# Kernel optimization log

Measured on AMD Instinct MI355X. Metric: run time of the kernel, lower is better.

## Reference

```python
import jax, jax.numpy as jnp
import numpy as np

B, NPG = 128, 128          # graphs, nodes per graph
N = B * NPG                # total nodes
K = 16                     # kNN neighbors within cutoff
D = 256                    # embedding_depth
H, DH = 4, 32              # heads = num_layers, head dim = (D//2)//H
L = 4                      # num graph convolutions
NR = 50                    # num_radial
CUTOFF = 2.0
OUT = 3 + 100              # 3 + max_ntypes


def setup_inputs() -> dict:
    rng = np.random.default_rng(0)
    pos = rng.standard_normal((N, 3)).astype(np.float32)
    nbrs = np.zeros((N, K), np.int32)
    mask = np.zeros((N, K), np.float32)
    for g in range(B):  # per-graph kNN with radial cutoff (setup only, numpy)
        p = pos[g * NPG:(g + 1) * NPG]
        d2 = ((p[:, None, :] - p[None, :, :]) ** 2).sum(-1)
        np.fill_diagonal(d2, np.inf)
        idx = np.argsort(d2, axis=1)[:, :K]
        dk = np.sqrt(np.take_along_axis(d2, idx, 1))
        nbrs[g * NPG:(g + 1) * NPG] = idx + g * NPG
        mask[g * NPG:(g + 1) * NPG] = (dk <= CUTOFF).astype(np.float32)
    batch_idx = np.repeat(np.arange(B, dtype=np.int32), NPG)

    key = jax.random.key(0)
    ks = jax.random.split(key, 12)
    s = 0.02
    return {
        'encoding': jax.random.normal(ks[0], (B, D), jnp.float32),
        'pos': jnp.asarray(pos),
        'batch_idx': jnp.asarray(batch_idx),
        'neighbors': jnp.asarray(nbrs),
        'nbr_mask': jnp.asarray(mask),
        'W_in': jax.random.normal(ks[1], (D + 3, D), jnp.float32) * s,
        'b_in': jnp.zeros((D,), jnp.float32),
        'Wq': jax.random.normal(ks[2], (L, D, H * DH), jnp.float32) * s,
        'Wk': jax.random.normal(ks[3], (L, D, H * DH), jnp.float32) * s,
        'Wv': jax.random.normal(ks[4], (L, D, H * DH), jnp.float32) * s,
        'We': jax.random.normal(ks[5], (L, NR, H * DH), jnp.float32) * s,
        'Wo': jax.random.normal(ks[6], (L, H * DH, D), jnp.float32) * s,
        'bo': jnp.zeros((L, D), jnp.float32),
        'Wfc': jax.random.normal(ks[7], (L, D, D), jnp.float32) * s,
        'bfc': jnp.zeros((L, D), jnp.float32),
        'ln_g': jnp.ones((L, D), jnp.float32),
        'ln_b': jnp.zeros((L, D), jnp.float32),
        'W_out': jax.random.normal(ks[8], (D, OUT), jnp.float32) * s,
        'b_out': jnp.zeros((OUT,), jnp.float32),
    }


def reference(encoding, pos, batch_idx, neighbors, nbr_mask,
              W_in, b_in, Wq, Wk, Wv, We, Wo, bo, Wfc, bfc,
              ln_g, ln_b, W_out, b_out):
    # x = encoding.repeat_interleave(graph_sizes); x[:, 0] = 1
    x = encoding[batch_idx]                      # [N, D]
    x = x.at[:, 0].set(1.0)
    h = jnp.concatenate([x, pos], axis=-1) @ W_in + b_in   # concat pos, embed

    # gaussian radial basis of neighbor distances
    dvec = pos[neighbors] - pos[:, None, :]      # [N, K, 3]
    d = jnp.sqrt((dvec ** 2).sum(-1) + 1e-12)    # [N, K]
    centers = jnp.linspace(0.0, CUTOFF, NR)
    width = centers[1] - centers[0]
    rbf = jnp.exp(-0.5 * ((d[..., None] - centers) / width) ** 2)  # [N, K, NR]

    scale = 1.0 / jnp.sqrt(jnp.float32(DH))
    m = nbr_mask[..., None]                      # [N, K, 1]
    for l in range(L):                           # TransformerConv layers
        q = (h @ Wq[l]).reshape(N, H, DH)
        k = (h @ Wk[l]).reshape(N, H, DH)
        v = (h @ Wv[l]).reshape(N, H, DH)
        e = (rbf @ We[l]).reshape(N, K, H, DH)   # edge embedding
        kj = k[neighbors] + e                    # [N, K, H, DH]
        vj = v[neighbors] + e
        logits = jnp.einsum('nhd,nkhd->nkh', q, kj) * scale
        logits = jnp.where(m > 0, logits, -1e9)
        a = jax.nn.softmax(logits, axis=1) * m   # masked attention over K
        msg = jnp.einsum('nkh,nkhd->nhd', a, vj).reshape(N, H * DH)
        h = h + msg @ Wo[l] + bo[l]              # residual update
        mu = h.mean(-1, keepdims=True)
        var = h.var(-1, keepdims=True)
        h = ln_g[l] * (h - mu) / jnp.sqrt(var + 1e-5) + ln_b[l]
        h = jax.nn.gelu(h @ Wfc[l] + bfc[l])     # nodewise fc (1 layer)

    return h @ W_out + b_out                     # [N, 3 + max_ntypes]
```

## Files before the change

### kernel.cpp

```cpp
#include <hip/hip_runtime.h>
#include <hip/hip_bf16.h>
#include <math.h>

#define N_PTS 16384
#define NLAYER 4

typedef __attribute__((ext_vector_type(8))) short bfrag;
typedef __attribute__((ext_vector_type(4))) float f32x4;
typedef __attribute__((ext_vector_type(4))) unsigned short u16x4;
typedef unsigned short ushort_t;
typedef unsigned int uint_t;

__device__ __forceinline__ ushort_t f2b(float f) {
  __hip_bfloat16 h = __float2bfloat16(f);
  return *reinterpret_cast<const ushort_t*>(&h);
}
__device__ __forceinline__ float b2f(ushort_t u) {
  union { uint_t i; float f; } c; c.i = ((uint_t)u) << 16; return c.f;
}
__device__ __forceinline__ float blo(uint_t u) {
  union { uint_t i; float f; } c; c.i = u << 16; return c.f;
}
__device__ __forceinline__ float bhi(uint_t u) {
  union { uint_t i; float f; } c; c.i = u & 0xffff0000u; return c.f;
}

__global__ __launch_bounds__(256) void base_kernel(
    const float* __restrict__ enc, const float* __restrict__ W_in,
    const float* __restrict__ b_in, float* __restrict__ base)
{
  int b = blockIdx.x, j = threadIdx.x;
  __shared__ float se[256];
  se[j] = enc[b * 256 + j];
  __syncthreads();
  float acc = b_in[j] + W_in[j];
  for (int i = 1; i < 256; ++i) acc += se[i] * W_in[i * 256 + j];
  base[b * 256 + j] = acc;
}

__global__ __launch_bounds__(256) void embed_kernel(
    const float* __restrict__ base, const int* __restrict__ batch_idx,
    const float* __restrict__ pos, const float* __restrict__ W_in,
    float* __restrict__ h, ushort_t* __restrict__ h_bf)
{
  int n = blockIdx.x, j = threadIdx.x;
  int b = batch_idx[n];
  float px = pos[n * 3 + 0], py = pos[n * 3 + 1], pz = pos[n * 3 + 2];
  float v = base[b * 256 + j]
      + px * W_in[256 * 256 + j] + py * W_in[257 * 256 + j] + pz * W_in[258 * 256 + j];
  h[(size_t)n * 256 + j] = v;
  h_bf[(size_t)n * 256 + j] = f2b(v);
}

__global__ __launch_bounds__(256) void prep_qkv(
    const float* __restrict__ Wq, const float* __restrict__ Wk,
    const float* __restrict__ Wv, const float* __restrict__ We,
    ushort_t* __restrict__ out)
{
  int idx = blockIdx.x * 256 + threadIdx.x;
  int l = idx / (640 * 256);
  int rem = idx - l * (640 * 256);
  int j = rem >> 8, k = rem & 255;
  float v = 0.f;
  if (j < 128) v = Wq[((size_t)l * 256 + k) * 128 + j];
  else if (j < 328) {
    int p = j - 128, hq = p / 50, r = p - hq * 50;
    const float* wq = &Wq[((size_t)l * 256 + k) * 128 + hq * 32];
    const float* we = &We[((size_t)l * 50 + r) * 128 + hq * 32];
#pragma unroll
    for (int d = 0; d < 32; ++d) v += wq[d] * we[d];
  } else if (j < 456) v = Wk[((size_t)l * 256 + k) * 128 + (j - 328)];
  else if (j < 584) v = Wv[((size_t)l * 256 + k) * 128 + (j - 456)];
  out[idx] = f2b(v);
}

__global__ __launch_bounds__(256) void prep_bcat(
    const float* __restrict__ We, const float* __restrict__ Wo, ushort_t* __restrict__ out)
{
  int idx = blockIdx.x * 256 + threadIdx.x;
  if (idx >= 4 * 256 * 352) return;
  int l = idx / (256 * 352);
  int rem = idx - l * (256 * 352);
  int j = rem / 352, k2 = rem - j * 352;
  float v = 0.f;
  if (k2 < 128) v = Wo[((size_t)l * 128 + k2) * 256 + j];
  else if (k2 < 328) {
    int p = k2 - 128, hq = p / 50, r = p - hq * 50;
    const float* we = &We[((size_t)l * 50 + r) * 128 + hq * 32];
    const float* wo = &Wo[((size_t)l * 128 + hq * 32) * 256 + j];
#pragma unroll
    for (int d = 0; d < 32; ++d) v += we[d] * wo[(size_t)d * 256];
  }
  out[idx] = f2b(v);
}

__global__ __launch_bounds__(256) void prep_wfc(
    const float* __restrict__ Wfc, ushort_t* __restrict__ out)
{
  int idx = blockIdx.x * 256 + threadIdx.x;
  int l = idx >> 16, rem = idx & 65535;
  int j = rem >> 8, k = rem & 255;
  out[idx] = f2b(Wfc[((size_t)l * 256 + k) * 256 + j]);
}

__global__ __launch_bounds__(256) void prep_wout(
    const float* __restrict__ W_out, ushort_t* __restrict__ out)
{
  int idx = blockIdx.x * 256 + threadIdx.x;
  int j = idx >> 8, k = idx & 255;
  out[idx] = (j < 103) ? f2b(W_out[(size_t)k * 103 + j]) : (ushort_t)0;
}

template<int EPI>
__global__ __launch_bounds__(256) void gemm_bf16(
    const ushort_t* __restrict__ A, const ushort_t* __restrict__ BT,
    const float* __restrict__ bias, const float* __restrict__ resid,
    float* __restrict__ Cf, ushort_t* __restrict__ Cb, ushort_t* __restrict__ Cb2,
    int K)
{
  __shared__ __align__(16) short As[128 * 40];
  __shared__ __align__(16) short Bs[64 * 40];
  const int tid = threadIdx.x;
  const int m0 = blockIdx.x * 128, n0 = blockIdx.y * 64;
  const int lane = tid & 63, wv = tid >> 6;
  const int wm = wv >> 1, wn = wv & 1;
  const int l15 = lane & 15, l4 = lane >> 4;
  const int asr = tid >> 1, asc = tid & 1;
  const int bsr = tid >> 2, bsc = tid & 3;

  f32x4 acc[4][2];
#pragma unroll
  for (int i = 0; i < 4; ++i)
#pragma unroll
    for (int j = 0; j < 2; ++j) acc[i][j] = (f32x4){0.f, 0.f, 0.f, 0.f};

  const ushort_t* gA = A + (size_t)(m0 + asr) * K + asc * 16;
  const ushort_t* gB = BT + (size_t)(n0 + bsr) * K + bsc * 8;
  short* wAs = As + asr * 40 + asc * 16;
  short* wBs = Bs + bsr * 40 + bsc * 8;

  for (int k0 = 0; k0 < K; k0 += 32) {
    *(bfrag*)wAs       = *(const bfrag*)(gA + k0);
    *(bfrag*)(wAs + 8) = *(const bfrag*)(gA + k0 + 8);
    *(bfrag*)wBs       = *(const bfrag*)(gB + k0);
    __syncthreads();
    bfrag af[4], bf[2];
#pragma unroll
    for (int m = 0; m < 4; ++m)
      af[m] = *(const bfrag*)(As + (wm * 64 + m * 16 + l15) * 40 + l4 * 8);
#pragma unroll
    for (int nn = 0; nn < 2; ++nn)
      bf[nn] = *(const bfrag*)(Bs + (wn * 32 + nn * 16 + l15) * 40 + l4 * 8);
#pragma unroll
    for (int m = 0; m < 4; ++m)
#pragma unroll
      for (int nn = 0; nn < 2; ++nn)
        acc[m][nn] = __builtin_amdgcn_mfma_f32_16x16x32_bf16(af[m], bf[nn], acc[m][nn], 0, 0, 0);
    __syncthreads();
  }

#pragma unroll
  for (int m = 0; m < 4; ++m) {
    const int rbase = m0 + wm * 64 + m * 16 + l4 * 4;
#pragma unroll
    for (int nn = 0; nn < 2; ++nn) {
      const int c = n0 + wn * 32 + nn * 16 + l15;
#pragma unroll
      for (int i = 0; i < 4; ++i) {
        const int r = rbase + i;
        float v = acc[m][nn][i];
        if (EPI == 0) {
          if (c < 328) Cb[(size_t)r * 328 + c] = f2b(v);
          else if (c < 584) Cb2[(size_t)r * 256 + (c - 328)] = f2b(v);
        } else if (EPI == 1) {
          if (c < 103) Cf[(size_t)r * 103 + c] = v + bias[c];
        } else if (EPI == 2) {
          Cf[(size_t)r * 256 + c] = v + bias[c] + resid[(size_t)r * 256 + c];
        } else {
          float x = v + bias[c];
          float t = tanhf(0.7978845608028654f * (x + 0.044715f * x * x * x));
          float gl = 0.5f * x * (1.f + t);
          Cf[(size_t)r * 256 + c] = gl;
          Cb[(size_t)r * 256 + c] = f2b(gl);
        }
      }
    }
  }
}

__global__ __launch_bounds__(512) void attn_kernel(
    const ushort_t* __restrict__ qext, const ushort_t* __restrict__ kvb,
    const float* __restrict__ pos, const int* __restrict__ nbrs,
    const float* __restrict__ mask, ushort_t* __restrict__ Amsg)
{
  __shared__ ushort_t sKV[128 * 264];
  __shared__ float sPos[128 * 3];
  __shared__ ushort_t sQ[8][336];
  __shared__ float sRbf[8][16][52];
  __shared__ float sA[8][64];
  __shared__ float sD[8][16];
  __shared__ float sMk[8][16];
  __shared__ int   sRn[8][16];

  const int tid = threadIdx.x;
  const int lane = tid & 63, w = tid >> 6;
  const int g = blockIdx.x >> 1, half = blockIdx.x & 1;
  const int base_pt = g * 128;

  for (int e = tid; e < 128 * 32; e += 512) {
    int r = e >> 5, c8 = e & 31;
    uint4 v = *(const uint4*)(kvb + ((size_t)(base_pt + r)) * 256 + c8 * 8);
    *(uint4*)(&sKV[r * 264 + c8 * 8]) = v;
  }
  for (int e = tid; e < 384; e += 512) sPos[e] = pos[(size_t)base_pt * 3 + e];
  __syncthreads();

  const int kk = lane >> 2, hh = lane & 3;
  for (int it = 0; it < 8; ++it) {
    const int rl = half * 64 + w * 8 + it;
    const int n = base_pt + rl;
    if (lane < 16) {
      int nb = nbrs[n * 16 + lane];
      int rn = nb - base_pt;
      sRn[w][lane] = rn;
      sMk[w][lane] = mask[n * 16 + lane];
      float dx = sPos[rn * 3 + 0] - sPos[rl * 3 + 0];
      float dy = sPos[rn * 3 + 1] - sPos[rl * 3 + 1];
      float dz = sPos[rn * 3 + 2] - sPos[rl * 3 + 2];
      sD[w][lane] = sqrtf(dx * dx + dy * dy + dz * dz + 1e-12f);
    }
    if (lane < 41)
      *(uint4*)(&sQ[w][lane * 8]) = *(const uint4*)(qext + (size_t)n * 328 + lane * 8);
    {
      int kk2 = lane & 15;
      float dk = sD[w][kk2];
      int r0 = lane >> 4;
#pragma unroll
      for (int j = 0; j < 13; ++j) {
        int r = r0 + j * 4;
        if (r < 50) {
          float t = (dk - (2.f / 49.f) * (float)r) * 24.5f;
          sRbf[w][kk2][r] = expf(-0.5f * t * t);
        }
      }
    }
    int rn = sRn[w][kk];
    const ushort_t* krow = &sKV[rn * 264 + hh * 32];
    float qk = 0.f;
#pragma unroll
    for (int c8 = 0; c8 < 4; ++c8) {
      uint4 kv4 = *(const uint4*)(krow + c8 * 8);
      const uint_t* q4 = (const uint_t*)(&sQ[w][hh * 32 + c8 * 8]);
      uint_t qa = q4[0], qb = q4[1], qc = q4[2], qd = q4[3];
      qk += blo(qa) * blo(kv4.x) + bhi(qa) * bhi(kv4.x)
          + blo(qb) * blo(kv4.y) + bhi(qb) * bhi(kv4.y)
          + blo(qc) * blo(kv4.z) + bhi(qc) * bhi(kv4.z)
          + blo(qd) * blo(kv4.w) + bhi(qd) * bhi(kv4.w);
    }
    float qe = 0.f;
#pragma unroll
    for (int r = 0; r < 50; ++r) qe += sRbf[w][kk][r] * b2f(sQ[w][128 + hh * 50 + r]);
    float lg = 0.17677669529663687f * (qk + qe);
    lg = (sMk[w][kk] > 0.f) ? lg : -1e9f;

    float mx = lg;
#pragma unroll
    for (int off = 4; off < 64; off <<= 1) mx = fmaxf(mx, __shfl_xor(mx, off, 64));
    float ex = expf(lg - mx);
    float sm = ex;
#pragma unroll
    for (int off = 4; off < 64; off <<= 1) sm += __shfl_xor(sm, off, 64);
    sA[w][kk * 4 + hh] = ex / sm * sMk[w][kk];

#pragma unroll
    for (int h2 = 0; h2 < 4; ++h2) {
      if (lane < 50) {
        float a2 = 0.f;
#pragma unroll
        for (int k2 = 0; k2 < 16; ++k2) a2 += sA[w][k2 * 4 + h2] * sRbf[w][k2][lane];
        Amsg[(size_t)n * 352 + 128 + h2 * 50 + lane] = f2b(a2);
      }
    }
#pragma unroll
    for (int hf = 0; hf < 2; ++hf) {
      int df = lane + hf * 64;
      int h2 = df >> 5;
      float a2 = 0.f;
#pragma unroll
      for (int k2 = 0; k2 < 16; ++k2)
        a2 += sA[w][k2 * 4 + h2] * b2f(sKV[sRn[w][k2] * 264 + 128 + df]);
      Amsg[(size_t)n * 352 + df] = f2b(a2);
    }
    if (lane < 24) Amsg[(size_t)n * 352 + 328 + lane] = 0;
  }
}

__global__ __launch_bounds__(256) void ln_bf(
    const float* __restrict__ h, const float* __restrict__ g,
    const float* __restrict__ b, ushort_t* __restrict__ out)
{
  int row = blockIdx.x * 4 + (threadIdx.x >> 6);
  int lane = threadIdx.x & 63;
  float4 x = *(const float4*)(h + (size_t)row * 256 + lane * 4);
  float s = x.x + x.y + x.z + x.w;
  float ss = x.x * x.x + x.y * x.y + x.z * x.z + x.w * x.w;
#pragma unroll
  for (int off = 1; off < 64; off <<= 1) {
    s += __shfl_xor(s, off, 64);
    ss += __shfl_xor(ss, off, 64);
  }
  float mu = s * (1.f / 256.f);
  float var = ss * (1.f / 256.f) - mu * mu;
  float inv = 1.0f / sqrtf(var + 1e-5f);
  float4 gg = *(const float4*)(g + lane * 4);
  float4 bb = *(const float4*)(b + lane * 4);
  u16x4 o;
  o.x = f2b(gg.x * (x.x - mu) * inv + bb.x);
  o.y = f2b(gg.y * (x.y - mu) * inv + bb.y);
  o.z = f2b(gg.z * (x.z - mu) * inv + bb.z);
  o.w = f2b(gg.w * (x.w - mu) * inv + bb.w);
  *(u16x4*)(out + (size_t)row * 256 + lane * 4) = o;
}

extern "C" void kernel_launch(void* const* d_in, const int* in_sizes, int n_in,
                              void* d_out, int out_size, void* d_ws, size_t ws_size,
                              hipStream_t stream) {
  const float* enc    = (const float*)d_in[0];
  const float* pos    = (const float*)d_in[1];
  const int*   bidx   = (const int*)  d_in[2];
  const int*   nbrs   = (const int*)  d_in[3];
  const float* mask   = (const float*)d_in[4];
  const float* W_in   = (const float*)d_in[5];
  const float* b_in   = (const float*)d_in[6];
  const float* Wq     = (const float*)d_in[7];
  const float* Wk     = (const float*)d_in[8];
  const float* Wv     = (const float*)d_in[9];
  const float* We     = (const float*)d_in[10];
  const float* Wo     = (const float*)d_in[11];
  const float* bo     = (const float*)d_in[12];
  const float* Wfc    = (const float*)d_in[13];
  const float* bfc    = (const float*)d_in[14];
  const float* ln_g   = (const float*)d_in[15];
  const float* ln_b   = (const float*)d_in[16];
  const float* W_out  = (const float*)d_in[17];
  const float* b_out  = (const float*)d_in[18];
  float* out = (float*)d_out;

  const int N = N_PTS;
  float* ws = (float*)d_ws;
  float*    h      = ws;
  ushort_t* qext_b = (ushort_t*)(h + (size_t)N * 256);
  ushort_t* kvb    = qext_b + (size_t)N * 328;
  ushort_t* hln    = kvb;
  ushort_t* h_bf   = kvb + (size_t)N * 256;
  ushort_t* Amsg   = h_bf + (size_t)N * 256;
  float*    base   = (float*)(Amsg + (size_t)N * 352);
  ushort_t* WqkvT  = (ushort_t*)(base + 128 * 256);
  ushort_t* BcT    = WqkvT + 4 * 640 * 256;
  ushort_t* WfT    = BcT  + 4 * 256 * 352;
  ushort_t* WoT    = WfT  + 4 * 256 * 256;

  base_kernel<<<128, 256, 0, stream>>>(enc, W_in, b_in, base);
  embed_kernel<<<N, 256, 0, stream>>>(base, bidx, pos, W_in, h, h_bf);
  prep_qkv<<<(4 * 640 * 256) / 256, 256, 0, stream>>>(Wq, Wk, Wv, We, WqkvT);
  prep_bcat<<<(4 * 256 * 352 + 255) / 256, 256, 0, stream>>>(We, Wo, BcT);
  prep_wfc<<<(4 * 256 * 256) / 256, 256, 0, stream>>>(Wfc, WfT);
  prep_wout<<<(128 * 256) / 256, 256, 0, stream>>>(W_out, WoT);

  for (int l = 0; l < NLAYER; ++l) {
    const ushort_t* WqkvT_l = WqkvT + (size_t)l * 640 * 256;
    const ushort_t* BcT_l   = BcT   + (size_t)l * 256 * 352;
    const ushort_t* WfT_l   = WfT   + (size_t)l * 256 * 256;
    const float* bo_l  = bo  + (size_t)l * 256;
    const float* bfc_l = bfc + (size_t)l * 256;
    const float* lg_l  = ln_g + (size_t)l * 256;
    const float* lb_l  = ln_b + (size_t)l * 256;

    gemm_bf16<0><<<dim3(N / 128, 10), 256, 0, stream>>>(
        h_bf, WqkvT_l, nullptr, nullptr, nullptr, qext_b, kvb, 256);

    attn_kernel<<<256, 512, 0, stream>>>(qext_b, kvb, pos, nbrs, mask, Amsg);

    gemm_bf16<2><<<dim3(N / 128, 4), 256, 0, stream>>>(
        Amsg, BcT_l, bo_l, h, h, nullptr, nullptr, 352);

    ln_bf<<<N / 4, 256, 0, stream>>>(h, lg_l, lb_l, hln);

    gemm_bf16<3><<<dim3(N / 128, 4), 256, 0, stream>>>(
        hln, WfT_l, bfc_l, nullptr, h, h_bf, nullptr, 256);
  }

  gemm_bf16<1><<<dim3(N / 128, 2), 256, 0, stream>>>(
      h_bf, WoT, b_out, nullptr, out, nullptr, nullptr, 256);
}
```

Before: 401.2 us.

## Widen GEMM tiles with direct-to-LDS loads and restructure attention into two phases

The GEMM now uses 128x128 tiles with global_load_lds 16-byte loads straight into unpadded shared memory, halving grid columns so each A tile is reused across more output columns. The attention kernel is split across four blocks per graph, staging K first and then V in a smaller shared buffer, and stores RBF values in bf16. It also uses fast __expf and vectorized q·e dot products. Larger per-block LDS reuse is traded against fewer blocks, unpadded LDS rows that may cause bank conflicts, and bf16 rounding of the RBF terms.

```diff
diff --git a/kernel.cpp b/kernel.cpp
--- a/kernel.cpp
+++ b/kernel.cpp
@@ -23,6 +23,12 @@
 }
 __device__ __forceinline__ float bhi(uint_t u) {
   union { uint_t i; float f; } c; c.i = u & 0xffff0000u; return c.f;
+}
+
+__device__ __forceinline__ void gload16(const ushort_t* g, ushort_t* l) {
+  __builtin_amdgcn_global_load_lds(
+      (const __attribute__((address_space(1))) unsigned int*)g,
+      (__attribute__((address_space(3))) unsigned int*)l, 16, 0, 0);
 }
 
 __global__ __launch_bounds__(256) void base_kernel(
@@ -118,43 +124,48 @@
     float* __restrict__ Cf, ushort_t* __restrict__ Cb, ushort_t* __restrict__ Cb2,
     int K)
 {
-  __shared__ __align__(16) short As[128 * 40];
-  __shared__ __align__(16) short Bs[64 * 40];
+  __shared__ __align__(16) ushort_t As[128 * 32];
+  __shared__ __align__(16) ushort_t Bs[128 * 32];
   const int tid = threadIdx.x;
-  const int m0 = blockIdx.x * 128, n0 = blockIdx.y * 64;
+  const int m0 = blockIdx.x * 128, n0 = blockIdx.y * 128;
   const int lane = tid & 63, wv = tid >> 6;
   const int wm = wv >> 1, wn = wv & 1;
   const int l15 = lane & 15, l4 = lane >> 4;
-  const int asr = tid >> 1, asc = tid & 1;
-  const int bsr = tid >> 2, bsc = tid & 3;
-
-  f32x4 acc[4][2];
+
+  const int srow = wv * 16 + (lane >> 2);
+  const int skc = (lane & 3) << 3;
+  const ushort_t* gA0 = A + (size_t)(m0 + srow) * K + skc;
+  const ushort_t* gA1 = gA0 + (size_t)64 * K;
+  const ushort_t* gB0 = BT + (size_t)(n0 + srow) * K + skc;
+  const ushort_t* gB1 = gB0 + (size_t)64 * K;
+  ushort_t* lA0 = As + wv * 512;
+  ushort_t* lA1 = As + 2048 + wv * 512;
+  ushort_t* lB0 = Bs + wv * 512;
+  ushort_t* lB1 = Bs + 2048 + wv * 512;
+
+  f32x4 acc[4][4];
 #pragma unroll
   for (int i = 0; i < 4; ++i)
 #pragma unroll
-    for (int j = 0; j < 2; ++j) acc[i][j] = (f32x4){0.f, 0.f, 0.f, 0.f};
-
-  const ushort_t* gA = A + (size_t)(m0 + asr) * K + asc * 16;
-  const ushort_t* gB = BT + (size_t)(n0 + bsr) * K + bsc * 8;
-  short* wAs = As + asr * 40 + asc * 16;
-  short* wBs = Bs + bsr * 40 + bsc * 8;
+    for (int j = 0; j < 4; ++j) acc[i][j] = (f32x4){0.f, 0.f, 0.f, 0.f};
 
   for (int k0 = 0; k0 < K; k0 += 32) {
-    *(bfrag*)wAs       = *(const bfrag*)(gA + k0);
-    *(bfrag*)(wAs + 8) = *(const bfrag*)(gA + k0 + 8);
-    *(bfrag*)wBs       = *(const bfrag*)(gB + k0);
+    gload16(gA0 + k0, lA0);
+    gload16(gA1 + k0, lA1);
+    gload16(gB0 + k0, lB0);
+    gload16(gB1 + k0, lB1);
     __syncthreads();
-    bfrag af[4], bf[2];
+    bfrag af[4], bf[4];
 #pragma unroll
     for (int m = 0; m < 4; ++m)
-      af[m] = *(const bfrag*)(As + (wm * 64 + m * 16 + l15) * 40 + l4 * 8);
-#pragma unroll
-    for (int nn = 0; nn < 2; ++nn)
-      bf[nn] = *(const bfrag*)(Bs + (wn * 32 + nn * 16 + l15) * 40 + l4 * 8);
+      af[m] = *(const bfrag*)(As + (wm * 64 + m * 16 + l15) * 32 + l4 * 8);
+#pragma unroll
+    for (int nn = 0; nn < 4; ++nn)
+      bf[nn] = *(const bfrag*)(Bs + (wn * 64 + nn * 16 + l15) * 32 + l4 * 8);
 #pragma unroll
     for (int m = 0; m < 4; ++m)
 #pragma unroll
-      for (int nn = 0; nn < 2; ++nn)
+      for (int nn = 0; nn < 4; ++nn)
         acc[m][nn] = __builtin_amdgcn_mfma_f32_16x16x32_bf16(af[m], bf[nn], acc[m][nn], 0, 0, 0);
     __syncthreads();
   }
@@ -163,8 +174,8 @@
   for (int m = 0; m < 4; ++m) {
     const int rbase = m0 + wm * 64 + m * 16 + l4 * 4;
 #pragma unroll
-    for (int nn = 0; nn < 2; ++nn) {
-      const int c = n0 + wn * 32 + nn * 16 + l15;
+    for (int nn = 0; nn < 4; ++nn) {
+      const int c = n0 + wn * 64 + nn * 16 + l15;
 #pragma unroll
       for (int i = 0; i < 4; ++i) {
         const int r = rbase + i;
@@ -193,44 +204,58 @@
     const float* __restrict__ pos, const int* __restrict__ nbrs,
     const float* __restrict__ mask, ushort_t* __restrict__ Amsg)
 {
-  __shared__ ushort_t sKV[128 * 264];
-  __shared__ float sPos[128 * 3];
-  __shared__ ushort_t sQ[8][336];
-  __shared__ float sRbf[8][16][52];
-  __shared__ float sA[8][64];
-  __shared__ float sD[8][16];
-  __shared__ float sMk[8][16];
-  __shared__ int   sRn[8][16];
+  __shared__ ushort_t sKV[128 * 136];
+  __shared__ float    sPos[384];
+  __shared__ float    sA[32][64];
+  __shared__ int      sRnAll[32][16];
+  __shared__ ushort_t sQ[8][128];
+  __shared__ float    sQE[8][4][52];
+  __shared__ ushort_t sRbf[8][16][52];
+  __shared__ float    sD[8][16];
+  __shared__ float    sMk[8][16];
 
   const int tid = threadIdx.x;
   const int lane = tid & 63, w = tid >> 6;
-  const int g = blockIdx.x >> 1, half = blockIdx.x & 1;
+  const int g = blockIdx.x & 127, q = blockIdx.x >> 7;
   const int base_pt = g * 128;
-
-  for (int e = tid; e < 128 * 32; e += 512) {
-    int r = e >> 5, c8 = e & 31;
-    uint4 v = *(const uint4*)(kvb + ((size_t)(base_pt + r)) * 256 + c8 * 8);
-    *(uint4*)(&sKV[r * 264 + c8 * 8]) = v;
+  const int kk = lane >> 2, hh = lane & 3;
+
+  for (int e = tid; e < 128 * 16; e += 512) {
+    int r = e >> 4, c8 = e & 15;
+    *(uint4*)(&sKV[r * 136 + c8 * 8]) =
+        *(const uint4*)(kvb + (size_t)(base_pt + r) * 256 + c8 * 8);
   }
   for (int e = tid; e < 384; e += 512) sPos[e] = pos[(size_t)base_pt * 3 + e];
   __syncthreads();
 
-  const int kk = lane >> 2, hh = lane & 3;
-  for (int it = 0; it < 8; ++it) {
-    const int rl = half * 64 + w * 8 + it;
+  for (int it = 0; it < 4; ++it) {
+    const int pt = w * 4 + it;
+    const int rl = q * 32 + pt;
     const int n = base_pt + rl;
     if (lane < 16) {
       int nb = nbrs[n * 16 + lane];
       int rn = nb - base_pt;
-      sRn[w][lane] = rn;
+      sRnAll[pt][lane] = rn;
       sMk[w][lane] = mask[n * 16 + lane];
       float dx = sPos[rn * 3 + 0] - sPos[rl * 3 + 0];
       float dy = sPos[rn * 3 + 1] - sPos[rl * 3 + 1];
       float dz = sPos[rn * 3 + 2] - sPos[rl * 3 + 2];
       sD[w][lane] = sqrtf(dx * dx + dy * dy + dz * dz + 1e-12f);
-    }
-    if (lane < 41)
+      sRbf[w][lane][50] = 0; sRbf[w][lane][51] = 0;
+    }
+    if (lane < 16)
       *(uint4*)(&sQ[w][lane * 8]) = *(const uint4*)(qext + (size_t)n * 328 + lane * 8);
+    if (lane < 50) {
+      uint2 u = *(const uint2*)(qext + (size_t)n * 328 + 128 + lane * 4);
+      int p = lane * 4;
+#pragma unroll
+      for (int e = 0; e < 4; ++e) {
+        ushort_t bb = ((const ushort_t*)&u)[e];
+        int pp = p + e, h2 = pp / 50, r = pp - h2 * 50;
+        sQE[w][h2][r] = b2f(bb);
+      }
+    }
+    if (lane < 8) sQE[w][lane >> 1][50 + (lane & 1)] = 0.f;
     {
       int kk2 = lane & 15;
       float dk = sD[w][kk2];
@@ -240,12 +265,12 @@
         int r = r0 + j * 4;
         if (r < 50) {
           float t = (dk - (2.f / 49.f) * (float)r) * 24.5f;
-          sRbf[w][kk2][r] = expf(-0.5f * t * t);
+          sRbf[w][kk2][r] = f2b(__expf(-0.5f * t * t));
         }
       }
     }
-    int rn = sRn[w][kk];
-    const ushort_t* krow = &sKV[rn * 264 + hh * 32];
+    int rn = sRnAll[pt][kk];
+    const ushort_t* krow = &sKV[rn * 136 + hh * 32];
     float qk = 0.f;
 #pragma unroll
     for (int c8 = 0; c8 < 4; ++c8) {
@@ -259,38 +284,65 @@
     }
     float qe = 0.f;
 #pragma unroll
-    for (int r = 0; r < 50; ++r) qe += sRbf[w][kk][r] * b2f(sQ[w][128 + hh * 50 + r]);
+    for (int c = 0; c < 13; ++c) {
+      float4 qv = *(const float4*)(&sQE[w][hh][c * 4]);
+      uint2 rv = *(const uint2*)(&sRbf[w][kk][c * 4]);
+      qe += qv.x * blo(rv.x) + qv.y * bhi(rv.x)
+          + qv.z * blo(rv.y) + qv.w * bhi(rv.y);
+    }
     float lg = 0.17677669529663687f * (qk + qe);
     lg = (sMk[w][kk] > 0.f) ? lg : -1e9f;
 
     float mx = lg;
 #pragma unroll
     for (int off = 4; off < 64; off <<= 1) mx = fmaxf(mx, __shfl_xor(mx, off, 64));
-    float ex = expf(lg - mx);
+    float ex = __expf(lg - mx);
     float sm = ex;
 #pragma unroll
     for (int off = 4; off < 64; off <<= 1) sm += __shfl_xor(sm, off, 64);
-    sA[w][kk * 4 + hh] = ex / sm * sMk[w][kk];
-
-#pragma unroll
-    for (int h2 = 0; h2 < 4; ++h2) {
-      if (lane < 50) {
-        float a2 = 0.f;
-#pragma unroll
-        for (int k2 = 0; k2 < 16; ++k2) a2 += sA[w][k2 * 4 + h2] * sRbf[w][k2][lane];
-        Amsg[(size_t)n * 352 + 128 + h2 * 50 + lane] = f2b(a2);
+    float a = ex / sm * sMk[w][kk];
+    sA[pt][kk * 4 + hh] = a;
+
+    if (lane < 50) {
+      float r0 = 0.f, r1 = 0.f, r2 = 0.f, r3 = 0.f;
+#pragma unroll
+      for (int k2 = 0; k2 < 16; ++k2) {
+        float rb = b2f(sRbf[w][k2][lane]);
+        r0 += sA[pt][k2 * 4 + 0] * rb;
+        r1 += sA[pt][k2 * 4 + 1] * rb;
+        r2 += sA[pt][k2 * 4 + 2] * rb;
+        r3 += sA[pt][k2 * 4 + 3] * rb;
       }
-    }
-#pragma unroll
-    for (int hf = 0; hf < 2; ++hf) {
-      int df = lane + hf * 64;
-      int h2 = df >> 5;
-      float a2 = 0.f;
-#pragma unroll
-      for (int k2 = 0; k2 < 16; ++k2)
-        a2 += sA[w][k2 * 4 + h2] * b2f(sKV[sRn[w][k2] * 264 + 128 + df]);
-      Amsg[(size_t)n * 352 + df] = f2b(a2);
-    }
+      Amsg[(size_t)n * 352 + 128 + 0 * 50 + lane] = f2b(r0);
+      Amsg[(size_t)n * 352 + 128 + 1 * 50 + lane] = f2b(r1);
+      Amsg[(size_t)n * 352 + 128 + 2 * 50 + lane] = f2b(r2);
+      Amsg[(size_t)n * 352 + 128 + 3 * 50 + lane] = f2b(r3);
+    }
+  }
+  __syncthreads();
+
+  for (int e = tid; e < 128 * 16; e += 512) {
+    int r = e >> 4, c8 = e & 15;
+    *(uint4*)(&sKV[r * 136 + c8 * 8]) =
+        *(const uint4*)(kvb + (size_t)(base_pt + r) * 256 + 128 + c8 * 8);
+  }
+  __syncthreads();
+
+  for (int it = 0; it < 4; ++it) {
+    const int pt = w * 4 + it;
+    const int n = base_pt + q * 32 + pt;
+    const int h2 = lane >> 4;
+    float m0 = 0.f, m1 = 0.f;
+#pragma unroll
+    for (int k2 = 0; k2 < 16; ++k2) {
+      int rn = sRnAll[pt][k2];
+      uint_t vv = *(const uint_t*)(&sKV[rn * 136 + lane * 2]);
+      float a = sA[pt][k2 * 4 + h2];
+      m0 += a * blo(vv);
+      m1 += a * bhi(vv);
+    }
+    uint_t o = (uint_t)f2b(m0) | ((uint_t)f2b(m1) << 16);
+    *(uint_t*)(&Amsg[(size_t)n * 352 + lane * 2]) = o;
     if (lane < 24) Amsg[(size_t)n * 352 + 328 + lane] = 0;
   }
 }
@@ -376,20 +428,20 @@
     const float* lg_l  = ln_g + (size_t)l * 256;
     const float* lb_l  = ln_b + (size_t)l * 256;
 
-    gemm_bf16<0><<<dim3(N / 128, 10), 256, 0, stream>>>(
+    gemm_bf16<0><<<dim3(N / 128, 5), 256, 0, stream>>>(
         h_bf, WqkvT_l, nullptr, nullptr, nullptr, qext_b, kvb, 256);
 
-    attn_kernel<<<256, 512, 0, stream>>>(qext_b, kvb, pos, nbrs, mask, Amsg);
-
-    gemm_bf16<2><<<dim3(N / 128, 4), 256, 0, stream>>>(
+    attn_kernel<<<512, 512, 0, stream>>>(qext_b, kvb, pos, nbrs, mask, Amsg);
+
+    gemm_bf16<2><<<dim3(N / 128, 2), 256, 0, stream>>>(
         Amsg, BcT_l, bo_l, h, h, nullptr, nullptr, 352);
 
     ln_bf<<<N / 4, 256, 0, stream>>>(h, lg_l, lb_l, hln);
 
-    gemm_bf16<3><<<dim3(N / 128, 4), 256, 0, stream>>>(
+    gemm_bf16<3><<<dim3(N / 128, 2), 256, 0, stream>>>(
         hln, WfT_l, bfc_l, nullptr, h, h_bf, nullptr, 256);
   }
 
-  gemm_bf16<1><<<dim3(N / 128, 2), 256, 0, stream>>>(
+  gemm_bf16<1><<<dim3(N / 128, 1), 256, 0, stream>>>(
       h_bf, WoT, b_out, nullptr, out, nullptr, nullptr, 256);
 }
```

Measured after the change: 409.1 us. Within noise of the previous version (+2.0%).
